# Kernel optimization log

Hardware: AMD Instinct MI355X
Metric: run time of the kernel (lower is better)

Reference implementation:

```python
import jax, jax.numpy as jnp
import numpy as np

N_NODES = 50000
N_EDGES = 250000
T_POOL = 4
C = 300


def setup_inputs() -> dict:
    key = jax.random.key(0)
    ks = jax.random.split(key, 7)
    x = jax.random.normal(ks[0], (N_NODES, T_POOL, C), dtype=jnp.float32)
    # edges guaranteed non-self-loop (so remove_self_loops is a no-op)
    row = jax.random.randint(ks[1], (N_EDGES,), 0, N_NODES, dtype=jnp.int32)
    off = jax.random.randint(ks[2], (N_EDGES,), 1, N_NODES, dtype=jnp.int32)
    col = (row + off) % N_NODES
    edge_index = jnp.stack([row, col], axis=0)
    W1 = jax.random.normal(ks[3], (300, C), dtype=jnp.float32) * 0.05
    b1 = jax.random.normal(ks[4], (300,), dtype=jnp.float32) * 0.05
    W2 = jax.random.normal(ks[5], (300, 300), dtype=jnp.float32) * 0.05
    b2 = jax.random.normal(ks[6], (300,), dtype=jnp.float32) * 0.05
    return {"x": x, "edge_index": edge_index, "W1": W1, "b1": b1, "W2": W2, "b2": b2}


def reference(x, edge_index, W1, b1, W2, b2):
    N = x.shape[0]
    row, col = edge_index[0], edge_index[1]
    # add self loops (input edges contain no self loops)
    sl = jnp.arange(N, dtype=row.dtype)
    row = jnp.concatenate([row, sl])
    col = jnp.concatenate([col, sl])
    # symmetric sqrt-degree norm, degree computed on source (row)
    deg = jax.ops.segment_sum(jnp.ones(row.shape[0], dtype=x.dtype), row, num_segments=N)
    dis = deg ** -0.5  # [N]

    def prop(h):  # out[i] = dis[i] * sum_{e: col_e=i} dis[row_e] * h[row_e]
        msg = (dis[:, None] * h)[row]  # [E+N, d]
        return dis[:, None] * jax.ops.segment_sum(msg, col, num_segments=N)

    # layer 1: linear -> mean pool over dim 1 -> propagate -> leaky_relu
    h = jnp.mean(jnp.einsum('ntc,oc->nto', x, W1) + b1, axis=1)  # [N, 300]
    h = jax.nn.leaky_relu(prop(h), negative_slope=0.01)
    # layer 2: linear -> propagate
    h2 = h @ W2.T + b2  # [N, out]
    return prop(h2)
```

## Files before the change

### kernel.cpp

```cpp
#include <hip/hip_runtime.h>

typedef __attribute__((ext_vector_type(8))) short bf16x8;
typedef __attribute__((ext_vector_type(4))) float f32x4;

__device__ __forceinline__ unsigned short f2bf(float f) {
    union { float f; unsigned u; } v; v.f = f;
    unsigned r = (v.u + 0x7FFFu + ((v.u >> 16) & 1u)) >> 16;
    return (unsigned short)r;
}
__device__ __forceinline__ unsigned pack2bf(float a, float b) {
    return (unsigned)f2bf(a) | ((unsigned)f2bf(b) << 16);
}
__device__ __forceinline__ float bflo(unsigned u) { union { unsigned u; float f; } v; v.u = u << 16; return v.f; }
__device__ __forceinline__ float bfhi(unsigned u) { union { unsigned u; float f; } v; v.u = u & 0xffff0000u; return v.f; }

__global__ void pool_kernel(const float* __restrict__ x, unsigned short* __restrict__ xm,
                            int N, int Mpad) {
    int tid = blockIdx.x * 256 + threadIdx.x;
    if (tid >= Mpad * 40) return;
    int n = tid / 40, k8 = tid % 40;
    int k = k8 * 8;
    float v[8] = {0.f,0.f,0.f,0.f,0.f,0.f,0.f,0.f};
    if (n < N && k < 300) {
        const float* xp = x + (size_t)n * 1200 + k;
        #pragma unroll
        for (int t = 0; t < 4; ++t) {
            const float4 lo = *(const float4*)(xp + t * 300);
            v[0] += lo.x; v[1] += lo.y; v[2] += lo.z; v[3] += lo.w;
            if (k + 4 < 300) {
                const float4 hi = *(const float4*)(xp + t * 300 + 4);
                v[4] += hi.x; v[5] += hi.y; v[6] += hi.z; v[7] += hi.w;
            }
        }
    }
    union { unsigned short u[8]; bf16x8 vec; } p;
    #pragma unroll
    for (int j = 0; j < 8; ++j) p.u[j] = f2bf(v[j] * 0.25f);
    *(bf16x8*)(xm + (size_t)tid * 8) = p.vec;
}

__global__ void setup_kernel(const float* __restrict__ W1, const float* __restrict__ b1,
                             const float* __restrict__ W2, const float* __restrict__ b2,
                             unsigned short* __restrict__ Ws1, unsigned short* __restrict__ Ws2,
                             float* __restrict__ bp1, float* __restrict__ bp2,
                             int* __restrict__ deg, int* __restrict__ cnt, int* __restrict__ cur,
                             int* __restrict__ total, int N) {
    int tid = blockIdx.x * 256 + threadIdx.x;
    if (tid == 0) *total = 0;
    if (tid < N) { deg[tid] = 0; cnt[tid] = 0; cur[tid] = 0; }
    if (tid < 304 * 320) {
        int c = tid / 320, k = tid % 320;
        int ks = k / 32, kk = k % 32;
        int cp  = c * 4 + (kk >> 3);
        int cps = cp ^ (c & 7);
        int dst = ks * 9728 + cps * 8 + (kk & 7);
        bool in = (c < 300) && (k < 300);
        Ws1[dst] = f2bf(in ? W1[c * 300 + k] : 0.f);
        Ws2[dst] = f2bf(in ? W2[c * 300 + k] : 0.f);
        if (tid < 304) { bp1[tid] = tid < 300 ? b1[tid] : 0.f; bp2[tid] = tid < 300 ? b2[tid] : 0.f; }
    }
}

__global__ void degcnt_kernel(const int* __restrict__ ei, int E,
                              int* __restrict__ deg, int* __restrict__ cnt) {
    int e = blockIdx.x * 256 + threadIdx.x;
    if (e >= E) return;
    atomicAdd(&deg[ei[e]], 1);
    atomicAdd(&cnt[ei[E + e]], 1);
}

__global__ void bucket_kernel(const int* __restrict__ cnt, const int* __restrict__ deg,
                              int2* __restrict__ bkt, float* __restrict__ dis,
                              int* __restrict__ total, int N) {
    __shared__ int sm[256];
    __shared__ int sbase;
    int i = blockIdx.x * 256 + threadIdx.x;
    int c = (i < N) ? cnt[i] : 0;
    sm[threadIdx.x] = c; __syncthreads();
    for (int off = 1; off < 256; off <<= 1) {
        int u = (threadIdx.x >= off) ? sm[threadIdx.x - off] : 0;
        __syncthreads();
        sm[threadIdx.x] += u;
        __syncthreads();
    }
    if (threadIdx.x == 255) sbase = atomicAdd(total, sm[255]);
    __syncthreads();
    if (i < N) {
        bkt[i] = make_int2(sbase + sm[threadIdx.x] - c, c);
        dis[i] = 1.0f / sqrtf((float)(deg[i] + 1));
    }
}

__global__ void fill_kernel(const int* __restrict__ ei, int E,
                            const int2* __restrict__ bkt, int* __restrict__ cur,
                            int* __restrict__ csr) {
    int e = blockIdx.x * 256 + threadIdx.x;
    if (e >= E) return;
    int r = ei[e], c = ei[E + e];
    int pos = bkt[c].x + atomicAdd(&cur[c], 1);
    csr[pos] = r;
}

__global__ __launch_bounds__(512, 4) void gemm_kernel(
    const unsigned short* __restrict__ A, const unsigned short* __restrict__ Ws,
    const float* __restrict__ bp, const float* __restrict__ dis,
    unsigned short* __restrict__ g, int N)
{
    __shared__ __align__(16) unsigned short lds[2][9728];
    const int t = threadIdx.x;
    const int lane = t & 63;
    const int wave = t >> 6;
    const int l15 = lane & 15, lhi = lane >> 4;
    const int rowBase = blockIdx.x * 128 + wave * 16;

    const unsigned short* Ap = A + (size_t)(rowBase + l15) * 320 + lhi * 8;
    const uint4* Wsrc = (const uint4*)Ws;

    const int rb16 = (l15 * 4 + lhi) ^ (l15 & 7);

    for (int grp = wave; grp < 19; grp += 8)
        __builtin_amdgcn_global_load_lds(
            (const __attribute__((address_space(1))) unsigned*)(Wsrc + grp * 64 + lane),
            (__attribute__((address_space(3))) unsigned*)(&lds[0][0] + grp * 512),
            16, 0, 0);

    bf16x8 a0 = *(const bf16x8*)(Ap);
    bf16x8 a1 = *(const bf16x8*)(Ap + 32);

    f32x4 acc[19];
    #pragma unroll
    for (int i = 0; i < 19; ++i) acc[i] = (f32x4){0.f,0.f,0.f,0.f};

    #pragma unroll
    for (int ks = 0; ks < 10; ++ks) {
        __syncthreads();
        if (ks < 9) {
            const uint4* s = Wsrc + (ks + 1) * 1216;
            unsigned short* d = &lds[(ks + 1) & 1][0];
            for (int grp = wave; grp < 19; grp += 8)
                __builtin_amdgcn_global_load_lds(
                    (const __attribute__((address_space(1))) unsigned*)(s + grp * 64 + lane),
                    (__attribute__((address_space(3))) unsigned*)(d + grp * 512),
                    16, 0, 0);
        }
        const unsigned short* lb = &lds[ks & 1][0] + rb16 * 8;
        #pragma unroll
        for (int cf = 0; cf < 19; ++cf) {
            bf16x8 b = *(const bf16x8*)(lb + cf * 512);
            acc[cf] = __builtin_amdgcn_mfma_f32_16x16x32_bf16(a0, b, acc[cf], 0, 0, 0);
        }
        a0 = a1;
        if (ks < 8) a1 = *(const bf16x8*)(Ap + (ks + 2) * 32);
    }

    const int n0 = rowBase + lhi * 4;
    float dd[4];
    #pragma unroll
    for (int r = 0; r < 4; ++r) dd[r] = (n0 + r < N) ? dis[n0 + r] : 0.f;
    #pragma unroll
    for (int cf = 0; cf < 19; ++cf) {
        int o = cf * 16 + l15;
        if (o < 300) {
            float bo = bp[o];
            #pragma unroll
            for (int r = 0; r < 4; ++r)
                if (n0 + r < N) g[(size_t)(n0 + r) * 320 + o] = f2bf(dd[r] * (acc[cf][r] + bo));
        }
    }
}

template<int MODE>
__global__ void prop_kernel(const unsigned short* __restrict__ g, const int2* __restrict__ bkt,
                            const int* __restrict__ csr, const float* __restrict__ dis,
                            void* __restrict__ outp, int N, int Mpad) {
    int wave = threadIdx.x >> 6;
    int lane = threadIdx.x & 63;
    int n = blockIdx.x * 4 + wave;
    if (n >= (MODE ? Mpad : N)) return;
    const bool act = lane < 38;
    float aL[4] = {0.f,0.f,0.f,0.f}, aH[4] = {0.f,0.f,0.f,0.f};
    if (n < N) {
        if (act) {
            uint4 u = *((const uint4*)(g + (size_t)n * 320) + lane);
            aL[0] = bflo(u.x); aH[0] = bfhi(u.x);
            aL[1] = bflo(u.y); aH[1] = bfhi(u.y);
            aL[2] = bflo(u.z); aH[2] = bfhi(u.z);
            aL[3] = bflo(u.w); aH[3] = bfhi(u.w);
        }
        int2 bk = bkt[n];
        int beg = bk.x, end = bk.x + bk.y;
        int j = beg;
        for (; j + 8 <= end; j += 8) {
            const uint4* q[8];
            #pragma unroll
            for (int m = 0; m < 8; ++m) q[m] = (const uint4*)(g + (size_t)csr[j + m] * 320) + lane;
            if (act) {
                #pragma unroll
                for (int m = 0; m < 8; ++m) {
                    uint4 u = *q[m];
                    aL[0] += bflo(u.x); aH[0] += bfhi(u.x);
                    aL[1] += bflo(u.y); aH[1] += bfhi(u.y);
                    aL[2] += bflo(u.z); aH[2] += bfhi(u.z);
                    aL[3] += bflo(u.w); aH[3] += bfhi(u.w);
                }
            }
        }
        for (; j + 4 <= end; j += 4) {
            int s0 = csr[j], s1 = csr[j+1], s2 = csr[j+2], s3 = csr[j+3];
            const uint4* p0 = (const uint4*)(g + (size_t)s0 * 320) + lane;
            const uint4* p1 = (const uint4*)(g + (size_t)s1 * 320) + lane;
            const uint4* p2 = (const uint4*)(g + (size_t)s2 * 320) + lane;
            const uint4* p3 = (const uint4*)(g + (size_t)s3 * 320) + lane;
            if (act) {
                uint4 u0 = *p0, u1 = *p1, u2 = *p2, u3 = *p3;
                aL[0] += bflo(u0.x) + bflo(u1.x) + bflo(u2.x) + bflo(u3.x);
                aH[0] += bfhi(u0.x) + bfhi(u1.x) + bfhi(u2.x) + bfhi(u3.x);
                aL[1] += bflo(u0.y) + bflo(u1.y) + bflo(u2.y) + bflo(u3.y);
                aH[1] += bfhi(u0.y) + bfhi(u1.y) + bfhi(u2.y) + bfhi(u3.y);
                aL[2] += bflo(u0.z) + bflo(u1.z) + bflo(u2.z) + bflo(u3.z);
                aH[2] += bfhi(u0.z) + bfhi(u1.z) + bfhi(u2.z) + bfhi(u3.z);
                aL[3] += bflo(u0.w) + bflo(u1.w) + bflo(u2.w) + bflo(u3.w);
                aH[3] += bfhi(u0.w) + bfhi(u1.w) + bfhi(u2.w) + bfhi(u3.w);
            }
        }
        for (; j < end; ++j) {
            const uint4* ps = (const uint4*)(g + (size_t)csr[j] * 320) + lane;
            if (act) {
                uint4 u = *ps;
                aL[0] += bflo(u.x); aH[0] += bfhi(u.x);
                aL[1] += bflo(u.y); aH[1] += bfhi(u.y);
                aL[2] += bflo(u.z); aH[2] += bfhi(u.z);
                aL[3] += bflo(u.w); aH[3] += bfhi(u.w);
            }
        }
        float dn = dis[n];
        #pragma unroll
        for (int i = 0; i < 4; ++i) { aL[i] *= dn; aH[i] *= dn; }
    }
    if (MODE == 0) {
        float* out = (float*)outp + (size_t)n * 300 + lane * 8;
        if (lane < 37) {
            float4 f0 = {aL[0], aH[0], aL[1], aH[1]};
            float4 f1 = {aL[2], aH[2], aL[3], aH[3]};
            *(float4*)out = f0;
            *(float4*)(out + 4) = f1;
        } else if (lane == 37) {
            float4 f0 = {aL[0], aH[0], aL[1], aH[1]};
            *(float4*)out = f0;
        }
    } else {
        uint4* h = (uint4*)((unsigned*)outp + (size_t)n * 160) + lane;
        if (lane < 40) {
            uint4 w = {0u, 0u, 0u, 0u};
            if (act) {
                float vL, vH;
                vL = aL[0]; vL = vL > 0.f ? vL : 0.01f * vL;
                vH = aH[0]; vH = vH > 0.f ? vH : 0.01f * vH;
                w.x = pack2bf(vL, vH);
                vL = aL[1]; vL = vL > 0.f ? vL : 0.01f * vL;
                vH = aH[1]; vH = vH > 0.f ? vH : 0.01f * vH;
                w.y = pack2bf(vL, vH);
                vL = aL[2]; vL = vL > 0.f ? vL : 0.01f * vL;
                vH = aH[2]; vH = vH > 0.f ? vH : 0.01f * vH;
                w.z = pack2bf(vL, vH);
                vL = aL[3]; vL = vL > 0.f ? vL : 0.01f * vL;
                vH = aH[3]; vH = vH > 0.f ? vH : 0.01f * vH;
                w.w = pack2bf(vL, vH);
                if (lane == 37) { w.z = 0u; w.w = 0u; }
            }
            *h = w;
        }
    }
}

extern "C" void kernel_launch(void* const* d_in, const int* in_sizes, int n_in,
                              void* d_out, int out_size, void* d_ws, size_t ws_size,
                              hipStream_t stream) {
    const float* x  = (const float*)d_in[0];
    const int*   ei = (const int*)d_in[1];
    const float* W1 = (const float*)d_in[2];
    const float* b1 = (const float*)d_in[3];
    const float* W2 = (const float*)d_in[4];
    const float* b2 = (const float*)d_in[5];
    float* out = (float*)d_out;

    const int N = in_sizes[0] / 1200;
    const int E = in_sizes[1] / 2;
    const int Mpad = ((N + 127) / 128) * 128;
    const int NB = (N + 255) / 256;

    char* p = (char*)d_ws;
    auto carve = [&](size_t bytes) -> char* {
        char* r = p; p += (bytes + 255) & ~(size_t)255; return r;
    };
    unsigned short* xm   = (unsigned short*)carve((size_t)Mpad * 320 * 2);
    unsigned short* g1   = (unsigned short*)carve((size_t)Mpad * 320 * 2);
    unsigned short* hb   = (unsigned short*)carve((size_t)Mpad * 320 * 2);
    unsigned short* g2   = (unsigned short*)carve((size_t)Mpad * 320 * 2);
    float* dis           = (float*)carve((size_t)N * 4);
    int* deg             = (int*)carve((size_t)N * 4);
    int* cnt             = (int*)carve((size_t)N * 4);
    int2* bkt            = (int2*)carve((size_t)N * 8);
    int* cur             = (int*)carve((size_t)N * 4);
    int* csr             = (int*)carve((size_t)E * 4);
    int* total           = (int*)carve(256);
    unsigned short* Ws1  = (unsigned short*)carve(304 * 320 * 2);
    unsigned short* Ws2  = (unsigned short*)carve(304 * 320 * 2);
    float* bp1           = (float*)carve(304 * 4);
    float* bp2           = (float*)carve(304 * 4);

    setup_kernel <<<(304 * 320 + 255) / 256, 256, 0, stream>>>(W1, b1, W2, b2, Ws1, Ws2, bp1, bp2,
                                                               deg, cnt, cur, total, N);
    pool_kernel  <<<(Mpad * 40 + 255) / 256, 256, 0, stream>>>(x, xm, N, Mpad);
    degcnt_kernel<<<(E + 255) / 256, 256, 0, stream>>>(ei, E, deg, cnt);
    bucket_kernel<<<NB, 256, 0, stream>>>(cnt, deg, bkt, dis, total, N);
    fill_kernel  <<<(E + 255) / 256, 256, 0, stream>>>(ei, E, bkt, cur, csr);

    gemm_kernel  <<<Mpad / 128, 512, 0, stream>>>(xm, Ws1, bp1, dis, g1, N);
    prop_kernel<1><<<Mpad / 4, 256, 0, stream>>>(g1, bkt, csr, dis, hb, N, Mpad);
    gemm_kernel  <<<Mpad / 128, 512, 0, stream>>>(hb, Ws2, bp2, dis, g2, N);
    prop_kernel<0><<<(N + 3) / 4, 256, 0, stream>>>(g2, bkt, csr, dis, out, N, Mpad);
}
```

Before: 259.7 us.

## Fuse mean-pooling of x into the first GEMM's A-operand load

Drops the separate pool kernel and its bf16 intermediate buffer. A new first-layer GEMM kernel reads fp32 x directly, averages over the 4 pooled slices in registers, converts to bf16 fragments, and prefetches the next K-slice alongside the weight tile copy into LDS. This removes one kernel launch and the write and re-read of the pooled intermediate. In exchange, the GEMM now streams the large fp32 input itself with only one stage of register prefetch, so memory latency may be less well hidden. The padded K columns also cause some reads past the end of each row.

Result: slower. 335.8 us (+29.3%).

```diff
diff --git a/kernel.cpp b/kernel.cpp
--- a/kernel.cpp
+++ b/kernel.cpp
@@ -13,31 +13,6 @@
 }
 __device__ __forceinline__ float bflo(unsigned u) { union { unsigned u; float f; } v; v.u = u << 16; return v.f; }
 __device__ __forceinline__ float bfhi(unsigned u) { union { unsigned u; float f; } v; v.u = u & 0xffff0000u; return v.f; }
-
-__global__ void pool_kernel(const float* __restrict__ x, unsigned short* __restrict__ xm,
-                            int N, int Mpad) {
-    int tid = blockIdx.x * 256 + threadIdx.x;
-    if (tid >= Mpad * 40) return;
-    int n = tid / 40, k8 = tid % 40;
-    int k = k8 * 8;
-    float v[8] = {0.f,0.f,0.f,0.f,0.f,0.f,0.f,0.f};
-    if (n < N && k < 300) {
-        const float* xp = x + (size_t)n * 1200 + k;
-        #pragma unroll
-        for (int t = 0; t < 4; ++t) {
-            const float4 lo = *(const float4*)(xp + t * 300);
-            v[0] += lo.x; v[1] += lo.y; v[2] += lo.z; v[3] += lo.w;
-            if (k + 4 < 300) {
-                const float4 hi = *(const float4*)(xp + t * 300 + 4);
-                v[4] += hi.x; v[5] += hi.y; v[6] += hi.z; v[7] += hi.w;
-            }
-        }
-    }
-    union { unsigned short u[8]; bf16x8 vec; } p;
-    #pragma unroll
-    for (int j = 0; j < 8; ++j) p.u[j] = f2bf(v[j] * 0.25f);
-    *(bf16x8*)(xm + (size_t)tid * 8) = p.vec;
-}
 
 __global__ void setup_kernel(const float* __restrict__ W1, const float* __restrict__ b1,
                              const float* __restrict__ W2, const float* __restrict__ b2,
@@ -101,6 +76,101 @@
     csr[pos] = r;
 }
 
+__global__ __launch_bounds__(512, 4) void gemm_x_kernel(
+    const float* __restrict__ x, const unsigned short* __restrict__ Ws,
+    const float* __restrict__ bp, const float* __restrict__ dis,
+    unsigned short* __restrict__ g, int N)
+{
+    __shared__ __align__(16) unsigned short lds[2][9728];
+    const int t = threadIdx.x;
+    const int lane = t & 63;
+    const int wave = t >> 6;
+    const int l15 = lane & 15, lhi = lane >> 4;
+    const int rowBase = blockIdx.x * 128 + wave * 16;
+    const int row = rowBase + l15;
+    const bool vrow = row < N;
+    const float* xp = x + (size_t)(vrow ? row : 0) * 1200;
+
+    const uint4* Wsrc = (const uint4*)Ws;
+    const int rb16 = (l15 * 4 + lhi) ^ (l15 & 7);
+    const f32x4 z4 = {0.f, 0.f, 0.f, 0.f};
+
+    f32x4 xs[8];
+    auto loadx = [&](int ks) {
+        int k0 = ks * 32 + lhi * 8;
+        bool half = vrow && (k0 < 300);
+        bool full = vrow && (k0 + 8 <= 300);
+        #pragma unroll
+        for (int tt = 0; tt < 4; ++tt) {
+            const float* q = xp + tt * 300 + k0;
+            f32x4 lo = *(const f32x4*)q;
+            f32x4 hi = *(const f32x4*)(q + 4);
+            xs[2 * tt]     = half ? lo : z4;
+            xs[2 * tt + 1] = full ? hi : z4;
+        }
+    };
+    auto makefrag = [&]() -> bf16x8 {
+        union { unsigned short u[8]; bf16x8 v; } pk;
+        #pragma unroll
+        for (int j = 0; j < 4; ++j) {
+            float sl = (xs[0][j] + xs[2][j]) + (xs[4][j] + xs[6][j]);
+            float sh = (xs[1][j] + xs[3][j]) + (xs[5][j] + xs[7][j]);
+            pk.u[j]     = f2bf(sl * 0.25f);
+            pk.u[4 + j] = f2bf(sh * 0.25f);
+        }
+        return pk.v;
+    };
+
+    loadx(0);
+    for (int grp = wave; grp < 19; grp += 8)
+        __builtin_amdgcn_global_load_lds(
+            (const __attribute__((address_space(1))) unsigned*)(Wsrc + grp * 64 + lane),
+            (__attribute__((address_space(3))) unsigned*)(&lds[0][0] + grp * 512),
+            16, 0, 0);
+    bf16x8 afrag = makefrag();
+
+    f32x4 acc[19];
+    #pragma unroll
+    for (int i = 0; i < 19; ++i) acc[i] = z4;
+
+    #pragma unroll
+    for (int ks = 0; ks < 10; ++ks) {
+        __syncthreads();
+        if (ks < 9) {
+            loadx(ks + 1);
+            const uint4* s = Wsrc + (ks + 1) * 1216;
+            unsigned short* d = &lds[(ks + 1) & 1][0];
+            for (int grp = wave; grp < 19; grp += 8)
+                __builtin_amdgcn_global_load_lds(
+                    (const __attribute__((address_space(1))) unsigned*)(s + grp * 64 + lane),
+                    (__attribute__((address_space(3))) unsigned*)(d + grp * 512),
+                    16, 0, 0);
+        }
+        const unsigned short* lb = &lds[ks & 1][0] + rb16 * 8;
+        #pragma unroll
+        for (int cf = 0; cf < 19; ++cf) {
+            bf16x8 b = *(const bf16x8*)(lb + cf * 512);
+            acc[cf] = __builtin_amdgcn_mfma_f32_16x16x32_bf16(afrag, b, acc[cf], 0, 0, 0);
+        }
+        if (ks < 9) afrag = makefrag();
+    }
+
+    const int n0 = rowBase + lhi * 4;
+    float dd[4];
+    #pragma unroll
+    for (int r = 0; r < 4; ++r) dd[r] = (n0 + r < N) ? dis[n0 + r] : 0.f;
+    #pragma unroll
+    for (int cf = 0; cf < 19; ++cf) {
+        int o = cf * 16 + l15;
+        if (o < 300) {
+            float bo = bp[o];
+            #pragma unroll
+            for (int r = 0; r < 4; ++r)
+                if (n0 + r < N) g[(size_t)(n0 + r) * 320 + o] = f2bf(dd[r] * (acc[cf][r] + bo));
+        }
+    }
+}
+
 __global__ __launch_bounds__(512, 4) void gemm_kernel(
     const unsigned short* __restrict__ A, const unsigned short* __restrict__ Ws,
     const float* __restrict__ bp, const float* __restrict__ dis,
@@ -115,7 +185,6 @@
 
     const unsigned short* Ap = A + (size_t)(rowBase + l15) * 320 + lhi * 8;
     const uint4* Wsrc = (const uint4*)Ws;
-
     const int rb16 = (l15 * 4 + lhi) ^ (l15 & 7);
 
     for (int grp = wave; grp < 19; grp += 8)
@@ -293,7 +362,6 @@
     auto carve = [&](size_t bytes) -> char* {
         char* r = p; p += (bytes + 255) & ~(size_t)255; return r;
     };
-    unsigned short* xm   = (unsigned short*)carve((size_t)Mpad * 320 * 2);
     unsigned short* g1   = (unsigned short*)carve((size_t)Mpad * 320 * 2);
     unsigned short* hb   = (unsigned short*)carve((size_t)Mpad * 320 * 2);
     unsigned short* g2   = (unsigned short*)carve((size_t)Mpad * 320 * 2);
@@ -311,12 +379,11 @@
 
     setup_kernel <<<(304 * 320 + 255) / 256, 256, 0, stream>>>(W1, b1, W2, b2, Ws1, Ws2, bp1, bp2,
                                                                deg, cnt, cur, total, N);
-    pool_kernel  <<<(Mpad * 40 + 255) / 256, 256, 0, stream>>>(x, xm, N, Mpad);
     degcnt_kernel<<<(E + 255) / 256, 256, 0, stream>>>(ei, E, deg, cnt);
     bucket_kernel<<<NB, 256, 0, stream>>>(cnt, deg, bkt, dis, total, N);
     fill_kernel  <<<(E + 255) / 256, 256, 0, stream>>>(ei, E, bkt, cur, csr);
 
-    gemm_kernel  <<<Mpad / 128, 512, 0, stream>>>(xm, Ws1, bp1, dis, g1, N);
+    gemm_x_kernel<<<Mpad / 128, 512, 0, stream>>>(x, Ws1, bp1, dis, g1, N);
     prop_kernel<1><<<Mpad / 4, 256, 0, stream>>>(g1, bkt, csr, dis, hb, N, Mpad);
     gemm_kernel  <<<Mpad / 128, 512, 0, stream>>>(hb, Ws2, bp2, dis, g2, N);
     prop_kernel<0><<<(N + 3) / 4, 256, 0, stream>>>(g2, bkt, csr, dis, out, N, Mpad);
```
